# Performance work log

Hardware: AMD Instinct MI355X
Metric: run time of the kernel (lower is better)

## Reference

```python
import jax, jax.numpy as jnp
import numpy as np

H = 1024
N_HEAD = 16
HEAD = H // N_HEAD
EPS = 1e-12


def setup_inputs() -> dict:
    key = jax.random.key(0)
    ks = jax.random.split(key, 12)
    B, S = 2, 2048
    scale = 1.0 / np.sqrt(H)
    inp = {
        "pre_out": jax.random.normal(ks[0], (B, S, H), dtype=jnp.float32),
        "att_mask": jnp.ones((B, 1, 1, S), dtype=jnp.float32),
        "Wq": jax.random.normal(ks[1], (H, H), dtype=jnp.float32) * scale,
        "bq": jnp.zeros((H,), dtype=jnp.float32),
        "Wk": jax.random.normal(ks[2], (H, H), dtype=jnp.float32) * scale,
        "bk": jnp.zeros((H,), dtype=jnp.float32),
        "Wv": jax.random.normal(ks[3], (H, H), dtype=jnp.float32) * scale,
        "bv": jnp.zeros((H,), dtype=jnp.float32),
        "Wo": jax.random.normal(ks[4], (H, H), dtype=jnp.float32) * scale,
        "bo": jnp.zeros((H,), dtype=jnp.float32),
        "ln_w": jnp.ones((H,), dtype=jnp.float32),
        "ln_b": jnp.zeros((H,), dtype=jnp.float32),
    }
    return inp


def _heads(x):
    # [B,S,H] -> [B,n_head,S,head]
    B, S, _ = x.shape
    return x.reshape(B, S, N_HEAD, HEAD).transpose(0, 2, 1, 3)


def _layernorm(x, w, b):
    u = jnp.mean(x, axis=-1, keepdims=True)
    s = jnp.mean((x - u) ** 2, axis=-1, keepdims=True)
    return w * ((x - u) / jnp.sqrt(s + EPS)) + b


def reference(pre_out, att_mask, Wq, bq, Wk, bk, Wv, bv, Wo, bo, ln_w, ln_b):
    B, S, _ = pre_out.shape
    # torch Linear: y = x @ W.T + b
    Q = _heads(pre_out @ Wq.T + bq)
    K = _heads(pre_out @ Wk.T + bk)
    V = _heads(pre_out @ Wv.T + bv)
    scores = jnp.einsum('bhqd,bhkd->bhqk', Q, K) / np.sqrt(HEAD)
    scores = scores + (1.0 - att_mask) * -10000.0
    prob = jax.nn.softmax(scores, axis=-1)  # eval mode: no dropout
    att = jnp.einsum('bhqk,bhkd->bhqd', prob, V)
    att = att.transpose(0, 2, 1, 3).reshape(B, S, H)
    out = att @ Wo.T + bo
    return _layernorm(pre_out + out, ln_w, ln_b)
```

## Files before the change

kernel.cpp:

```cpp
#include <hip/hip_runtime.h>
#include <math.h>

typedef unsigned short u16;
typedef float floatx4 __attribute__((ext_vector_type(4)));
typedef __bf16 bf16x8 __attribute__((ext_vector_type(8)));
typedef u16 u16x4 __attribute__((ext_vector_type(4)));

#define BB 2
#define SS 2048
#define HH 1024
#define NHEAD 16

__device__ __forceinline__ u16 f2bf(float f) {
  union { float f; unsigned u; } a; a.f = f;
  unsigned r = a.u + 0x7fffu + ((a.u >> 16) & 1u);
  return (u16)(r >> 16);
}

__device__ __forceinline__ u16 bfbits(float f) {
  union { __bf16 h; u16 u; } c; c.h = (__bf16)f; return c.u;
}

__device__ __forceinline__ unsigned cvtpk(float lo, float hi) {
  unsigned r;
  asm("v_cvt_pk_bf16_f32 %0, %1, %2" : "=v"(r) : "v"(lo), "v"(hi));
  return r;
}

__device__ __forceinline__ void gload16(const u16* g, u16* l) {
  __builtin_amdgcn_global_load_lds((const __attribute__((address_space(1))) void*)g,
                                   (__attribute__((address_space(3))) void*)l, 16, 0, 0);
}

__device__ __forceinline__ void fencebar() {
  asm volatile("" ::: "memory");
  __builtin_amdgcn_s_barrier();
  asm volatile("" ::: "memory");
}

__global__ __launch_bounds__(256) void cvt_all(
    const float* __restrict__ X, const float* __restrict__ Wq, const float* __restrict__ Wk,
    const float* __restrict__ Wv, const float* __restrict__ Wo, const float* __restrict__ mask,
    u16* __restrict__ Xb, u16* __restrict__ Wqb, u16* __restrict__ Wkb,
    u16* __restrict__ Wvb, u16* __restrict__ Wob, float* __restrict__ B2) {
  int i = blockIdx.x * 256 + threadIdx.x;
  if (i >= (2 << 20)) {
    int off = i - (2 << 20);
    float4 m = ((const float4*)mask)[off];
    float4 o;
    o.x = (1.0f - m.x) * (-10000.0f * 1.44269504f);
    o.y = (1.0f - m.y) * (-10000.0f * 1.44269504f);
    o.z = (1.0f - m.z) * (-10000.0f * 1.44269504f);
    o.w = (1.0f - m.w) * (-10000.0f * 1.44269504f);
    ((float4*)B2)[off] = o;
    return;
  }
  const float* src; u16* dst; int off;
  if (i < (1 << 20)) { src = X; dst = Xb; off = i; }
  else {
    int j = i - (1 << 20);
    int m = j >> 18; off = j & ((1 << 18) - 1);
    src = (m == 0) ? Wq : (m == 1) ? Wk : (m == 2) ? Wv : Wo;
    dst = (m == 0) ? Wqb : (m == 1) ? Wkb : (m == 2) ? Wvb : Wob;
  }
  float4 v = ((const float4*)src)[off];
  u16x4 p; p.x = f2bf(v.x); p.y = f2bf(v.y); p.z = f2bf(v.z); p.w = f2bf(v.w);
  ((u16x4*)dst)[off] = p;
}

__global__ __launch_bounds__(256) void qkv_gemm(
    const u16* __restrict__ X,
    const u16* __restrict__ Wq, const u16* __restrict__ Wk, const u16* __restrict__ Wv,
    const float* __restrict__ bq, const float* __restrict__ bk, const float* __restrict__ bv,
    u16* __restrict__ Qo, u16* __restrict__ Ko, u16* __restrict__ Vt) {
  __shared__ u16 As[2][128 * 32];
  __shared__ u16 Ws[2][128 * 32];

  const int tid = threadIdx.x;
  const int w = tid >> 6, lane = tid & 63, quad = lane >> 4, l15 = lane & 15;
  const int L = blockIdx.y * 24 + blockIdx.x;
  const int wid = (L & 7) * 96 + (L >> 3);
  const int bx = wid % 24, by = wid / 24;
  const int mat = bx >> 3;
  const int col0 = (bx & 7) * 128;
  const int row0 = by * 128;
  const u16* W = (mat == 0) ? Wq : (mat == 1) ? Wk : Wv;
  const float* bias = (mat == 0) ? bq : (mat == 1) ? bk : bv;

  const int c0 = tid, c1 = tid + 256;
  const int ar0 = c0 >> 2, al0 = ((c0 & 3) ^ (ar0 & 3)) * 8;
  const int ar1 = c1 >> 2, al1 = ((c1 & 3) ^ (ar1 & 3)) * 8;
  const u16* gA0 = X + (row0 + ar0) * HH + al0;
  const u16* gA1 = X + (row0 + ar1) * HH + al1;
  const u16* gW0 = W + (col0 + ar0) * HH + al0;
  const u16* gW1 = W + (col0 + ar1) * HH + al1;

  const int wm = (w >> 1) * 64, wn = (w & 1) * 64;
  const int sw = quad ^ (l15 & 3);
  const int aoff = (wm + l15) * 32 + sw * 8;
  const int boff = (wn + l15) * 32 + sw * 8;

  auto stage = [&](int buf, int k0) {
    gload16(gA0 + k0, As[buf] + c0 * 8);
    gload16(gA1 + k0, As[buf] + c1 * 8);
    gload16(gW0 + k0, Ws[buf] + c0 * 8);
    gload16(gW1 + k0, Ws[buf] + c1 * 8);
  };

  floatx4 acc[4][4];
#pragma unroll
  for (int i = 0; i < 4; i++)
#pragma unroll
    for (int j = 0; j < 4; j++) acc[i][j] = {0.f, 0.f, 0.f, 0.f};

  stage(0, 0);

  for (int kt = 0; kt < 32; kt++) {
    const int cur = kt & 1;
    if (kt < 31) {
      stage(cur ^ 1, (kt + 1) * 32);
      asm volatile("s_waitcnt vmcnt(4)" ::: "memory");
    } else {
      asm volatile("s_waitcnt vmcnt(0)" ::: "memory");
    }
    fencebar();

    bf16x8 af[4], bfr[4];
#pragma unroll
    for (int i = 0; i < 4; i++) af[i] = *(const bf16x8*)(As[cur] + aoff + i * 512);
#pragma unroll
    for (int j = 0; j < 4; j++) bfr[j] = *(const bf16x8*)(Ws[cur] + boff + j * 512);
    __builtin_amdgcn_s_setprio(1);
#pragma unroll
    for (int i = 0; i < 4; i++)
#pragma unroll
      for (int j = 0; j < 4; j++)
        acc[i][j] = __builtin_amdgcn_mfma_f32_16x16x32_bf16(af[i], bfr[j], acc[i][j], 0, 0, 0);
    __builtin_amdgcn_s_setprio(0);

    fencebar();
  }

  const int rb = row0 + wm + quad * 4;
  if (mat < 2) {
    u16* O = (mat == 0) ? Qo : Ko;
#pragma unroll
    for (int j = 0; j < 4; j++) {
      const int col = col0 + wn + j * 16 + l15;
      const float bj = bias[col];
#pragma unroll
      for (int i = 0; i < 4; i++) {
        const int r0 = rb + i * 16;
#pragma unroll
        for (int r = 0; r < 4; r++)
          O[(r0 + r) * HH + col] = bfbits(acc[i][j][r] + bj);
      }
    }
  } else {
#pragma unroll
    for (int j = 0; j < 4; j++) {
      const int col = col0 + wn + j * 16 + l15;
      const float bj = bias[col];
      const int h = col >> 6, d = col & 63;
#pragma unroll
      for (int i = 0; i < 4; i++) {
        const int m0 = rb + i * 16;
        const int b = m0 >> 11, s = m0 & 2047;
        u16x4 pk;
#pragma unroll
        for (int r = 0; r < 4; r++) pk[r] = bfbits(acc[i][j][r] + bj);
        *(u16x4*)(Vt + (((b * NHEAD + h) * 64 + d) * SS + s)) = pk;
      }
    }
  }
}

__global__ __launch_bounds__(256) void oproj_gemm(
    const u16* __restrict__ A, const u16* __restrict__ W,
    const float* __restrict__ bias, float* __restrict__ Y) {
  __shared__ u16 As[2][128 * 32];
  __shared__ u16 Ws[2][64 * 32];

  const int tid = threadIdx.x;
  const int w = tid >> 6, lane = tid & 63, quad = lane >> 4, l15 = lane & 15;
  const int L = blockIdx.y * 16 + blockIdx.x;
  const int wid = (L & 7) * 64 + (L >> 3);
  const int col0 = (wid & 15) * 64;
  const int row0 = (wid >> 4) * 128;

  const int c0 = tid, c1 = tid + 256;
  const int ar0 = c0 >> 2, al0 = ((c0 & 3) ^ (ar0 & 3)) * 8;
  const int ar1 = c1 >> 2, al1 = ((c1 & 3) ^ (ar1 & 3)) * 8;
  const u16* gA0 = A + (row0 + ar0) * HH + al0;
  const u16* gA1 = A + (row0 + ar1) * HH + al1;
  const u16* gW0 = W + (col0 + ar0) * HH + al0;

  const int wm = w * 32;
  const int sw = quad ^ (l15 & 3);
  const int aoff = (wm + l15) * 32 + sw * 8;
  const int boff = l15 * 32 + sw * 8;

  auto stage = [&](int buf, int k0) {
    gload16(gA0 + k0, As[buf] + c0 * 8);
    gload16(gA1 + k0, As[buf] + c1 * 8);
    gload16(gW0 + k0, Ws[buf] + c0 * 8);
  };

  floatx4 acc[2][4];
#pragma unroll
  for (int i = 0; i < 2; i++)
#pragma unroll
    for (int j = 0; j < 4; j++) acc[i][j] = {0.f, 0.f, 0.f, 0.f};

  stage(0, 0);

  for (int kt = 0; kt < 32; kt++) {
    const int cur = kt & 1;
    if (kt < 31) {
      stage(cur ^ 1, (kt + 1) * 32);
      asm volatile("s_waitcnt vmcnt(3)" ::: "memory");
    } else {
      asm volatile("s_waitcnt vmcnt(0)" ::: "memory");
    }
    fencebar();

    bf16x8 af[2], bfr[4];
#pragma unroll
    for (int i = 0; i < 2; i++) af[i] = *(const bf16x8*)(As[cur] + aoff + i * 512);
#pragma unroll
    for (int j = 0; j < 4; j++) bfr[j] = *(const bf16x8*)(Ws[cur] + boff + j * 512);
    __builtin_amdgcn_s_setprio(1);
#pragma unroll
    for (int i = 0; i < 2; i++)
#pragma unroll
      for (int j = 0; j < 4; j++)
        acc[i][j] = __builtin_amdgcn_mfma_f32_16x16x32_bf16(af[i], bfr[j], acc[i][j], 0, 0, 0);
    __builtin_amdgcn_s_setprio(0);

    fencebar();
  }

  const int rb = row0 + wm + quad * 4;
#pragma unroll
  for (int j = 0; j < 4; j++) {
    const int col = col0 + j * 16 + l15;
    const float bj = bias[col];
#pragma unroll
    for (int i = 0; i < 2; i++) {
      const int r0 = rb + i * 16;
#pragma unroll
      for (int r = 0; r < 4; r++)
        Y[(r0 + r) * HH + col] = acc[i][j][r] + bj;
    }
  }
}

#define QT 128

__global__ __launch_bounds__(512, 4) void attn_mfma(
    const u16* __restrict__ Q, const u16* __restrict__ K, const u16* __restrict__ Vt,
    const float* __restrict__ B2, u16* __restrict__ O) {
  __shared__ u16 SMEM[33024];
  u16* const KB = SMEM;
  u16* const VB = SMEM + 16384;

  const int L = blockIdx.y * 16 + blockIdx.x;
  const int wid = (L & 7) * 64 + (L >> 3);
  const int qt = wid & 15, bh = wid >> 4;
  const int b = bh >> 4, h = bh & 15;
  const int tid = threadIdx.x;
  const int w = tid >> 6, lane = tid & 63, quad = lane >> 4, l15 = lane & 15;
  const int sw = l15 & 7;
  const int qg = w & 3;
  const int khalf = w >> 2;
  const int koff = khalf * 32;

  const int qbase  = (b * SS + qt * QT) * HH + h * 64;
  const int kvbase = (b * SS) * HH + h * 64;
  const int vtbase = (b * NHEAD + h) * 64 * SS;

  auto stage_kv = [&](int bi, int t) {
    const int c = tid;
    const int r = c >> 3, lc = (c & 7) ^ (r & 7);
    gload16(K + kvbase + (t * 64 + r) * HH + lc * 8, KB + bi * 4096 + c * 8);
    gload16(Vt + vtbase + r * SS + t * 64 + lc * 8, VB + bi * 4096 + c * 8);
  };

  bf16x8 aQ[2][2];
#pragma unroll
  for (int mt = 0; mt < 2; mt++) {
    const u16* qr = Q + qbase + (qg * 32 + mt * 16 + l15) * HH;
    aQ[mt][0] = *(const bf16x8*)(qr + quad * 8);
    aQ[mt][1] = *(const bf16x8*)(qr + (4 + quad) * 8);
  }
  stage_kv(0, 0);
  stage_kv(1, 1);
  asm volatile("s_waitcnt vmcnt(2)" ::: "memory");

  floatx4 o[2][4];
#pragma unroll
  for (int mt = 0; mt < 2; mt++)
#pragma unroll
    for (int j = 0; j < 4; j++) o[mt][j] = {0.f, 0.f, 0.f, 0.f};
  float lp[2] = {0.f, 0.f};

  const float* B2row = B2 + b * SS;

  const int vc0 = khalf * 4 + (quad >> 1);
  const int vsub = (quad & 1) * 4;

  bf16x8 pa[2];

  for (int kt = 0; kt < 32; kt++) {
    fencebar();

    const float* B2k = B2row + kt * 64 + koff;
    floatx4 bb[2];
    bb[0] = *(const floatx4*)(B2k + quad * 4);
    bb[1] = *(const floatx4*)(B2k + 16 + quad * 4);
    asm volatile("" ::: "memory");

    if (kt < 30) {
      stage_kv((kt + 2) & 3, kt + 2);
      asm volatile("s_waitcnt vmcnt(2)" ::: "memory");
    } else {
      asm volatile("s_waitcnt vmcnt(0)" ::: "memory");
    }

    const u16* Kc = KB + (kt & 3) * 4096;

    floatx4 st[2][2];
    __builtin_amdgcn_s_setprio(1);
#pragma unroll
    for (int kb = 0; kb < 2; kb++) {
      const u16* kr = Kc + (koff + kb * 16 + l15) * 64;
      bf16x8 kf0 = *(const bf16x8*)(kr + ((quad ^ sw) * 8));
      bf16x8 kf1 = *(const bf16x8*)(kr + (((4 + quad) ^ sw) * 8));
#pragma unroll
      for (int mt = 0; mt < 2; mt++) {
        floatx4 z = {0.f, 0.f, 0.f, 0.f};
        z = __builtin_amdgcn_mfma_f32_16x16x32_bf16(kf0, aQ[mt][0], z, 0, 0, 0);
        st[mt][kb] = __builtin_amdgcn_mfma_f32_16x16x32_bf16(kf1, aQ[mt][1], z, 0, 0, 0);
      }
    }

    if (kt) {
      const u16* Vp = VB + ((kt - 1) & 3) * 4096;
#pragma unroll
      for (int j = 0; j < 4; j++) {
        const u16* vrow = Vp + (j * 16 + l15) * 64 + vsub;
        union { u16x4 hh[2]; bf16x8 v; } vu;
        vu.hh[0] = *(const u16x4*)(vrow + ((vc0 ^ sw) * 8));
        vu.hh[1] = *(const u16x4*)(vrow + (((vc0 + 2) ^ sw) * 8));
#pragma unroll
        for (int mt = 0; mt < 2; mt++)
          o[mt][j] = __builtin_amdgcn_mfma_f32_16x16x32_bf16(pa[mt], vu.v, o[mt][j], 0, 0, 0);
      }
    }
    __builtin_amdgcn_s_setprio(0);

#pragma unroll
    for (int mt = 0; mt < 2; mt++) {
      float pe[2][4];
#pragma unroll
      for (int kb = 0; kb < 2; kb++)
#pragma unroll
        for (int r = 0; r < 4; r++) {
          pe[kb][r] = __builtin_amdgcn_exp2f(st[mt][kb][r] * 0.180336880f + bb[kb][r]);
          lp[mt] += pe[kb][r];
        }
      union { unsigned wd[4]; bf16x8 v; } pu;
      pu.wd[0] = cvtpk(pe[0][0], pe[0][1]);
      pu.wd[1] = cvtpk(pe[0][2], pe[0][3]);
      pu.wd[2] = cvtpk(pe[1][0], pe[1][1]);
      pu.wd[3] = cvtpk(pe[1][2], pe[1][3]);
      pa[mt] = pu.v;
    }
  }

  {
    const u16* Vp = VB + (31 & 3) * 4096;
    __builtin_amdgcn_s_setprio(1);
#pragma unroll
    for (int j = 0; j < 4; j++) {
      const u16* vrow = Vp + (j * 16 + l15) * 64 + vsub;
      union { u16x4 hh[2]; bf16x8 v; } vu;
      vu.hh[0] = *(const u16x4*)(vrow + ((vc0 ^ sw) * 8));
      vu.hh[1] = *(const u16x4*)(vrow + (((vc0 + 2) ^ sw) * 8));
#pragma unroll
      for (int mt = 0; mt < 2; mt++)
        o[mt][j] = __builtin_amdgcn_mfma_f32_16x16x32_bf16(pa[mt], vu.v, o[mt][j], 0, 0, 0);
    }
    __builtin_amdgcn_s_setprio(0);
  }

  fencebar();

#pragma unroll
  for (int mt = 0; mt < 2; mt++) {
    float v = lp[mt];
    v += __shfl_xor(v, 16);
    v += __shfl_xor(v, 32);
    lp[mt] = v;
  }

  float* const oS  = (float*)SMEM;
  float* const lpS = (float*)(SMEM + 32768);
  if (w >= 4) {
    float* pb = oS + (w - 4) * 2048;
#pragma unroll
    for (int mt = 0; mt < 2; mt++) {
#pragma unroll
      for (int j = 0; j < 4; j++)
#pragma unroll
        for (int r = 0; r < 4; r++)
          pb[(mt * 16 + quad * 4 + r) * 64 + j * 16 + l15] = o[mt][j][r];
      if (quad == 0) lpS[qg * 32 + mt * 16 + l15] = lp[mt];
    }
  }
  asm volatile("s_waitcnt lgkmcnt(0)" ::: "memory");
  fencebar();

  if (w < 4) {
    const float* pb = oS + w * 2048;
    float lpt[2];
#pragma unroll
    for (int mt = 0; mt < 2; mt++)
      lpt[mt] = lp[mt] + lpS[w * 32 + mt * 16 + l15];
#pragma unroll
    for (int mt = 0; mt < 2; mt++) {
      const int orow0 = b * SS + qt * QT + qg * 32 + mt * 16 + quad * 4;
#pragma unroll
      for (int r = 0; r < 4; r++) {
        const float inv = 1.0f / __shfl(lpt[mt], quad * 4 + r);
#pragma unroll
        for (int j = 0; j < 4; j++) {
          const float val = o[mt][j][r] + pb[(mt * 16 + quad * 4 + r) * 64 + j * 16 + l15];
          O[(orow0 + r) * HH + h * 64 + j * 16 + l15] = bfbits(val * inv);
        }
      }
    }
  }
}

__global__ __launch_bounds__(256) void add_layernorm(
    const float* __restrict__ x0, const float* __restrict__ y,
    const float* __restrict__ w, const float* __restrict__ b,
    float* __restrict__ out) {
  const int row = blockIdx.x * 4 + (threadIdx.x >> 6);
  const int l = threadIdx.x & 63;
  const float4* xr = (const float4*)(x0 + (size_t)row * HH);
  const float4* yr = (const float4*)(y + (size_t)row * HH);

  float4 v[4];
  float s = 0.f;
#pragma unroll
  for (int i = 0; i < 4; i++) {
    const float4 a = xr[l + i * 64];
    const float4 c = yr[l + i * 64];
    v[i].x = a.x + c.x; v[i].y = a.y + c.y;
    v[i].z = a.z + c.z; v[i].w = a.w + c.w;
    s += v[i].x + v[i].y + v[i].z + v[i].w;
  }
#pragma unroll
  for (int o = 1; o < 64; o <<= 1) s += __shfl_xor(s, o);
  const float mean = s * (1.0f / HH);

  float sq = 0.f;
#pragma unroll
  for (int i = 0; i < 4; i++) {
    const float dx = v[i].x - mean, dy = v[i].y - mean;
    const float dz = v[i].z - mean, dw = v[i].w - mean;
    sq += dx * dx + dy * dy + dz * dz + dw * dw;
  }
#pragma unroll
  for (int o = 1; o < 64; o <<= 1) sq += __shfl_xor(sq, o);
  const float inv = rsqrtf(sq * (1.0f / HH) + 1e-12f);

  float4* orow = (float4*)(out + (size_t)row * HH);
#pragma unroll
  for (int i = 0; i < 4; i++) {
    const float4 ww = ((const float4*)w)[l + i * 64];
    const float4 bb = ((const float4*)b)[l + i * 64];
    float4 o4;
    o4.x = ww.x * ((v[i].x - mean) * inv) + bb.x;
    o4.y = ww.y * ((v[i].y - mean) * inv) + bb.y;
    o4.z = ww.z * ((v[i].z - mean) * inv) + bb.z;
    o4.w = ww.w * ((v[i].w - mean) * inv) + bb.w;
    orow[l + i * 64] = o4;
  }
}

extern "C" void kernel_launch(void* const* d_in, const int* in_sizes, int n_in,
                              void* d_out, int out_size, void* d_ws, size_t ws_size,
                              hipStream_t stream) {
  const float* pre_out = (const float*)d_in[0];
  const float* mask    = (const float*)d_in[1];
  const float* Wq = (const float*)d_in[2];
  const float* bq = (const float*)d_in[3];
  const float* Wk = (const float*)d_in[4];
  const float* bk = (const float*)d_in[5];
  const float* Wv = (const float*)d_in[6];
  const float* bv = (const float*)d_in[7];
  const float* Wo = (const float*)d_in[8];
  const float* bo = (const float*)d_in[9];
  const float* ln_w = (const float*)d_in[10];
  const float* ln_b = (const float*)d_in[11];
  float* out = (float*)d_out;

  u16* Xb  = (u16*)d_ws;
  u16* Wqb = Xb + (4 << 20);
  u16* Wkb = Wqb + (1 << 20);
  u16* Wvb = Wkb + (1 << 20);
  u16* Wob = Wvb + (1 << 20);
  u16* Qb  = Wob + (1 << 20);
  u16* Kb  = Qb + (4 << 20);
  u16* Vtb = Kb + (4 << 20);
  u16* Ab  = Vtb + (4 << 20);
  float* Yb = (float*)(Ab + (4 << 20));
  float* B2 = Yb + (4 << 20);

  cvt_all<<<8196, 256, 0, stream>>>(pre_out, Wq, Wk, Wv, Wo, mask,
                                    Xb, Wqb, Wkb, Wvb, Wob, B2);

  qkv_gemm<<<dim3(24, 32), 256, 0, stream>>>(Xb, Wqb, Wkb, Wvb, bq, bk, bv, Qb, Kb, Vtb);

  attn_mfma<<<dim3(SS / QT, BB * NHEAD), 512, 0, stream>>>(Qb, Kb, Vtb, B2, Ab);

  oproj_gemm<<<dim3(16, 32), 256, 0, stream>>>(Ab, Wob, bo, Yb);

  add_layernorm<<<BB * SS / 4, 256, 0, stream>>>(pre_out, Yb, ln_w, ln_b, out);
}
```

Measured before the change: 205.8 us.

## Shrink attention K/V ring to three stages and compute PV in-iteration

The K/V shared-memory ring in the attention kernel goes from four 64-key stages to three, and the occupancy hint in the launch bounds rises from 4 to 6 blocks. The PV product, which used to be deferred one iteration to overlap with the next QK step, now runs in the same iteration right after the softmax, so the post-loop epilogue goes away. Global and LDS address arithmetic is strength-reduced into pointers that advance each step and rotating buffer offsets. The smaller LDS footprint could allow more resident blocks, but the grid of 512 blocks may already fit. PV MFMAs now depend directly on the exp results, and the tighter register budget may force spills.

After: 307.2 us. 49.3% more time.

```diff
diff --git a/kernel.cpp b/kernel.cpp
--- a/kernel.cpp
+++ b/kernel.cpp
@@ -257,12 +257,12 @@
 
 #define QT 128
 
-__global__ __launch_bounds__(512, 4) void attn_mfma(
+__global__ __launch_bounds__(512, 6) void attn_mfma(
     const u16* __restrict__ Q, const u16* __restrict__ K, const u16* __restrict__ Vt,
     const float* __restrict__ B2, u16* __restrict__ O) {
-  __shared__ u16 SMEM[33024];
+  __shared__ u16 SMEM[24576];
   u16* const KB = SMEM;
-  u16* const VB = SMEM + 16384;
+  u16* const VB = SMEM + 12288;
 
   const int L = blockIdx.y * 16 + blockIdx.x;
   const int wid = (L & 7) * 64 + (L >> 3);
@@ -279,12 +279,9 @@
   const int kvbase = (b * SS) * HH + h * 64;
   const int vtbase = (b * NHEAD + h) * 64 * SS;
 
-  auto stage_kv = [&](int bi, int t) {
-    const int c = tid;
-    const int r = c >> 3, lc = (c & 7) ^ (r & 7);
-    gload16(K + kvbase + (t * 64 + r) * HH + lc * 8, KB + bi * 4096 + c * 8);
-    gload16(Vt + vtbase + r * SS + t * 64 + lc * 8, VB + bi * 4096 + c * 8);
-  };
+  const int sr = tid >> 3, slc = (tid & 7) ^ (sr & 7);
+  const u16* gKp = K + kvbase + sr * HH + slc * 8;
+  const u16* gVp = Vt + vtbase + sr * SS + slc * 8;
 
   bf16x8 aQ[2][2];
 #pragma unroll
@@ -293,8 +290,11 @@
     aQ[mt][0] = *(const bf16x8*)(qr + quad * 8);
     aQ[mt][1] = *(const bf16x8*)(qr + (4 + quad) * 8);
   }
-  stage_kv(0, 0);
-  stage_kv(1, 1);
+  gload16(gKp, KB + tid * 8);
+  gload16(gVp, VB + tid * 8);
+  gload16(gKp + 64 * HH, KB + 4096 + tid * 8);
+  gload16(gVp + 64, VB + 4096 + tid * 8);
+  gKp += 2 * 64 * HH; gVp += 2 * 64;
   asm volatile("s_waitcnt vmcnt(2)" ::: "memory");
 
   floatx4 o[2][4];
@@ -304,38 +304,44 @@
     for (int j = 0; j < 4; j++) o[mt][j] = {0.f, 0.f, 0.f, 0.f};
   float lp[2] = {0.f, 0.f};
 
-  const float* B2row = B2 + b * SS;
-
+  const float* B2p = B2 + b * SS + koff;
+
+  const int krow0 = (koff + l15) * 64;
+  const int kro0 = (quad ^ sw) * 8, kro1 = ((4 + quad) ^ sw) * 8;
   const int vc0 = khalf * 4 + (quad >> 1);
   const int vsub = (quad & 1) * 4;
-
-  bf16x8 pa[2];
+  const int vo0 = (vc0 ^ sw) * 8 + vsub, vo1 = ((vc0 + 2) ^ sw) * 8 + vsub;
+
+  int cOff = 0, nOff = 4096, sOff = 8192;
 
   for (int kt = 0; kt < 32; kt++) {
     fencebar();
 
-    const float* B2k = B2row + kt * 64 + koff;
     floatx4 bb[2];
-    bb[0] = *(const floatx4*)(B2k + quad * 4);
-    bb[1] = *(const floatx4*)(B2k + 16 + quad * 4);
+    bb[0] = *(const floatx4*)(B2p + quad * 4);
+    bb[1] = *(const floatx4*)(B2p + 16 + quad * 4);
+    B2p += 64;
     asm volatile("" ::: "memory");
 
     if (kt < 30) {
-      stage_kv((kt + 2) & 3, kt + 2);
+      gload16(gKp, KB + sOff + tid * 8);
+      gload16(gVp, VB + sOff + tid * 8);
+      gKp += 64 * HH; gVp += 64;
       asm volatile("s_waitcnt vmcnt(2)" ::: "memory");
     } else {
       asm volatile("s_waitcnt vmcnt(0)" ::: "memory");
     }
 
-    const u16* Kc = KB + (kt & 3) * 4096;
+    const u16* Kc = KB + cOff;
+    const u16* Vc = VB + cOff;
 
     floatx4 st[2][2];
     __builtin_amdgcn_s_setprio(1);
 #pragma unroll
     for (int kb = 0; kb < 2; kb++) {
-      const u16* kr = Kc + (koff + kb * 16 + l15) * 64;
-      bf16x8 kf0 = *(const bf16x8*)(kr + ((quad ^ sw) * 8));
-      bf16x8 kf1 = *(const bf16x8*)(kr + (((4 + quad) ^ sw) * 8));
+      const u16* kr = Kc + krow0 + kb * 1024;
+      bf16x8 kf0 = *(const bf16x8*)(kr + kro0);
+      bf16x8 kf1 = *(const bf16x8*)(kr + kro1);
 #pragma unroll
       for (int mt = 0; mt < 2; mt++) {
         floatx4 z = {0.f, 0.f, 0.f, 0.f};
@@ -343,22 +349,9 @@
         st[mt][kb] = __builtin_amdgcn_mfma_f32_16x16x32_bf16(kf1, aQ[mt][1], z, 0, 0, 0);
       }
     }
-
-    if (kt) {
-      const u16* Vp = VB + ((kt - 1) & 3) * 4096;
-#pragma unroll
-      for (int j = 0; j < 4; j++) {
-        const u16* vrow = Vp + (j * 16 + l15) * 64 + vsub;
-        union { u16x4 hh[2]; bf16x8 v; } vu;
-        vu.hh[0] = *(const u16x4*)(vrow + ((vc0 ^ sw) * 8));
-        vu.hh[1] = *(const u16x4*)(vrow + (((vc0 + 2) ^ sw) * 8));
-#pragma unroll
-        for (int mt = 0; mt < 2; mt++)
-          o[mt][j] = __builtin_amdgcn_mfma_f32_16x16x32_bf16(pa[mt], vu.v, o[mt][j], 0, 0, 0);
-      }
-    }
     __builtin_amdgcn_s_setprio(0);
 
+    bf16x8 pa[2];
 #pragma unroll
     for (int mt = 0; mt < 2; mt++) {
       float pe[2][4];
@@ -376,22 +369,21 @@
       pu.wd[3] = cvtpk(pe[1][2], pe[1][3]);
       pa[mt] = pu.v;
     }
-  }
-
-  {
-    const u16* Vp = VB + (31 & 3) * 4096;
+
     __builtin_amdgcn_s_setprio(1);
 #pragma unroll
     for (int j = 0; j < 4; j++) {
-      const u16* vrow = Vp + (j * 16 + l15) * 64 + vsub;
+      const u16* vrow = Vc + (j * 16 + l15) * 64;
       union { u16x4 hh[2]; bf16x8 v; } vu;
-      vu.hh[0] = *(const u16x4*)(vrow + ((vc0 ^ sw) * 8));
-      vu.hh[1] = *(const u16x4*)(vrow + (((vc0 + 2) ^ sw) * 8));
+      vu.hh[0] = *(const u16x4*)(vrow + vo0);
+      vu.hh[1] = *(const u16x4*)(vrow + vo1);
 #pragma unroll
       for (int mt = 0; mt < 2; mt++)
         o[mt][j] = __builtin_amdgcn_mfma_f32_16x16x32_bf16(pa[mt], vu.v, o[mt][j], 0, 0, 0);
     }
     __builtin_amdgcn_s_setprio(0);
+
+    const int t = cOff; cOff = nOff; nOff = sOff; sOff = t;
   }
 
   fencebar();
@@ -405,7 +397,7 @@
   }
 
   float* const oS  = (float*)SMEM;
-  float* const lpS = (float*)(SMEM + 32768);
+  float* const lpS = (float*)(SMEM + 16384);
   if (w >= 4) {
     float* pb = oS + (w - 4) * 2048;
 #pragma unroll
```
